# Performance work log

Hardware: AMD Instinct MI355X
Metric: run time of the kernel (lower is better)

## Reference

```python
import jax, jax.numpy as jnp
import numpy as np

L, H, M, KB = 8, 512, 32, 256  # layers, hidden, fourier modes, key bits
EPS = 1e-5


def setup_inputs() -> dict:
    key = jax.random.key(0)
    ks = jax.random.split(key, 20)
    B, S = 8, 2048
    s = 0.02
    return {
        'x': jax.random.normal(ks[0], (B, S), jnp.float32),
        # input projection Linear(1, H): weight [H] (squeezed), bias [H]
        'in_w': jax.random.normal(ks[1], (H,), jnp.float32) * s,
        'in_b': jax.random.normal(ks[2], (H,), jnp.float32) * s,
        # per-layer fourier weights (complex, stored as real/imag), conv1d(k=1), layernorm
        'fw_r': jax.random.normal(ks[3], (L, M, H, H), jnp.float32) * s,
        'fw_i': jax.random.normal(ks[4], (L, M, H, H), jnp.float32) * s,
        'conv_w': jax.random.normal(ks[5], (L, H, H), jnp.float32) / np.sqrt(H),
        'conv_b': jax.random.normal(ks[6], (L, H), jnp.float32) * s,
        'ln_g': jnp.ones((L, H), jnp.float32),
        'ln_b': jnp.zeros((L, H), jnp.float32),
        # output projection H -> H/2 -> H/4 -> 1
        'op1_w': jax.random.normal(ks[7], (H // 2, H), jnp.float32) / np.sqrt(H),
        'op1_b': jnp.zeros((H // 2,), jnp.float32),
        'op2_w': jax.random.normal(ks[8], (H // 4, H // 2), jnp.float32) / np.sqrt(H // 2),
        'op2_b': jnp.zeros((H // 4,), jnp.float32),
        'op3_w': jax.random.normal(ks[9], (1, H // 4), jnp.float32) / np.sqrt(H // 4),
        'op3_b': jnp.zeros((1,), jnp.float32),
        # cryptanalytic head H -> H -> KB (sigmoid)
        'h1_w': jax.random.normal(ks[10], (H, H), jnp.float32) / np.sqrt(H),
        'h1_b': jnp.zeros((H,), jnp.float32),
        'h2_w': jax.random.normal(ks[11], (KB, H), jnp.float32) / np.sqrt(H),
        'h2_b': jnp.zeros((KB,), jnp.float32),
    }


def _gelu(x):
    return jax.nn.gelu(x, approximate=False)


def _fourier_layer(x, Wc, cw, cb, g, b):
    # x: [B, S, H]; Wc: [M, H, H] complex
    S = x.shape[1]
    x_ft = jnp.fft.rfft(x, axis=1)  # [B, F, H] complex, F = S//2+1
    m = min(M, x_ft.shape[1])
    # batched per-mode complex GEMM (replaces python loop over modes)
    spec = jnp.einsum('bmh,mhk->bmk', x_ft[:, :m], Wc[:m])
    out_ft = jnp.concatenate([spec, jnp.zeros_like(x_ft[:, m:])], axis=1)
    x_fourier = jnp.fft.irfft(out_ft, n=S, axis=1)  # real [B, S, H]
    x_conv = x @ cw.T + cb  # Conv1d kernel-size-1 == per-position linear
    y = x_fourier + x_conv
    mu = jnp.mean(y, axis=-1, keepdims=True)
    var = jnp.var(y, axis=-1, keepdims=True)
    return (y - mu) * jax.lax.rsqrt(var + EPS) * g + b


def reference(x, in_w, in_b, fw_r, fw_i, conv_w, conv_b, ln_g, ln_b,
              op1_w, op1_b, op2_w, op2_b, op3_w, op3_b,
              h1_w, h1_b, h2_w, h2_b):
    # input projection: Linear(1, H) on x[..., None]
    h = x[:, :, None] * in_w[None, None, :] + in_b  # [B, S, H]
    Wc = fw_r + 1j * fw_i  # [L, M, H, H]
    for l in range(L):
        h = _fourier_layer(h, Wc[l], conv_w[l], conv_b[l], ln_g[l], ln_b[l]) + h
    # output projection (dropout is identity in eval)
    o = _gelu(h @ op1_w.T + op1_b)
    o = _gelu(o @ op2_w.T + op2_b)
    output = (o @ op3_w.T + op3_b)[..., 0]  # [B, S]
    gf = jnp.mean(h, axis=1)  # [B, H]
    k = _gelu(gf @ h1_w.T + h1_b)
    key_pred = jax.nn.sigmoid(k @ h2_w.T + h2_b)  # [B, KB]
    return output, key_pred
```

## Files before the change

### kernel.cpp

```cpp
#include <hip/hip_runtime.h>
#include <hip/hip_bf16.h>
#include <math.h>

#define BB   8
#define SEQ  2048
#define HD   512
#define LAY  8
#define MD   32
#define NKB  256
#define LNEPS 1e-5f

typedef __attribute__((ext_vector_type(8))) short v8s;
typedef __attribute__((ext_vector_type(4))) float v4f;
typedef __attribute__((ext_vector_type(4))) unsigned short v4us;

__device__ __forceinline__ float b2f(__hip_bfloat16 v) { return __bfloat162float(v); }
__device__ __forceinline__ float geluf(float v) { return v * 0.5f * (1.f + erff(v * 0.70710678118654752f)); }
__device__ __forceinline__ float bflo(unsigned int u) { return __uint_as_float((u & 0xFFFFu) << 16); }
__device__ __forceinline__ float bfhi(unsigned int u) { return __uint_as_float(u & 0xFFFF0000u); }

__device__ __forceinline__ float ldin(const void* p, size_t i, int bf) {
    if (bf) return __bfloat162float(((const __hip_bfloat16*)p)[i]);
    return ((const float*)p)[i];
}
__device__ __forceinline__ void stout(void* p, size_t i, float v, int bf) {
    if (bf) ((__hip_bfloat16*)p)[i] = __float2bfloat16(v);
    else    ((float*)p)[i] = v;
}

__device__ __forceinline__ void gl2lds16(const void* g, void* l) {
    __builtin_amdgcn_global_load_lds((__attribute__((address_space(1))) void*)g,
                                     (__attribute__((address_space(3))) void*)l, 16, 0, 0);
}

__global__ void k_flag(const unsigned int* __restrict__ lng_bits, int* __restrict__ flag) {
    if (threadIdx.x == 0 && blockIdx.x == 0)
        *flag = (lng_bits[0] == 0x3F803F80u) ? 1 : 0;
}

__global__ void k_setup(const void* __restrict__ x, const void* __restrict__ in_w, const void* __restrict__ in_b,
                        const void* __restrict__ cw, const void* __restrict__ w1, const void* __restrict__ w2,
                        const void* __restrict__ h1w, const void* __restrict__ h2w,
                        __hip_bfloat16* __restrict__ Ffwd, __hip_bfloat16* __restrict__ T2,
                        __hip_bfloat16* __restrict__ cwbf, __hip_bfloat16* __restrict__ w1bf,
                        __hip_bfloat16* __restrict__ w2bf, float* __restrict__ h1T, float* __restrict__ h2T,
                        float* __restrict__ h, __hip_bfloat16* __restrict__ hbf,
                        float* __restrict__ Xft, float* __restrict__ gf,
                        const int* __restrict__ flag) {
    int bf = *flag;
    int blk = blockIdx.x, t = threadIdx.x;
    if (blk < 512) {
        int idx = blk * 256 + t;
        int j = idx >> 11, s = idx & 2047;
        int m = j >> 1;
        int phase = (m * s) & (SEQ - 1);
        float ang = (float)phase * (6.283185307179586f / (float)SEQ);
        Ffwd[idx] = __float2bfloat16((j & 1) ? -sinf(ang) : cosf(ang));
    } else if (blk < 1024) {
        int idx = (blk - 512) * 256 + t;
        int s = idx >> 6, j = idx & 63;
        int m = j >> 1;
        float v;
        if (j == 0)      v = 1.f / (float)SEQ;
        else if (j == 1) v = 0.f;
        else {
            int phase = (m * s) & (SEQ - 1);
            float ang = (float)phase * (6.283185307179586f / (float)SEQ);
            v = (j & 1) ? (-2.f / (float)SEQ) * sinf(ang) : (2.f / (float)SEQ) * cosf(ang);
        }
        T2[idx] = __float2bfloat16(v);
    } else if (blk < 9216) {
        int idx = (blk - 1024) * 256 + t;
        cwbf[idx] = __float2bfloat16(ldin(cw, idx, bf));
    } else if (blk < 9728) {
        int idx = (blk - 9216) * 256 + t;
        w1bf[idx] = __float2bfloat16(ldin(w1, idx, bf));
    } else if (blk < 9856) {
        int idx = (blk - 9728) * 256 + t;
        w2bf[idx] = __float2bfloat16(ldin(w2, idx, bf));
    } else if (blk < 10880) {
        int idx = (blk - 9856) * 256 + t;
        int r = idx & 511, c = idx >> 9;
        h1T[idx] = ldin(h1w, (size_t)r * 512 + c, bf);
    } else if (blk < 11392) {
        int idx = (blk - 10880) * 256 + t;
        int r = idx & 255, c = idx >> 8;
        h2T[idx] = ldin(h2w, (size_t)r * 512 + c, bf);
    } else if (blk < 12416) {
        int idx = (blk - 11392) * 256 + t;
        Xft[idx] = 0.f;
    } else if (blk < 12432) {
        int idx = (blk - 12416) * 256 + t;
        gf[idx] = 0.f;
    } else {
        int idx = (blk - 12432) * 256 + t;
        int j = idx & 511;
        int bs = idx >> 9;
        float v = ldin(x, bs, bf) * ldin(in_w, j, bf) + ldin(in_b, j, bf);
        h[idx] = v;
        hbf[idx] = __float2bfloat16(v);
    }
}

__global__ __launch_bounds__(256) void k_fdft2(const __hip_bfloat16* __restrict__ hbf,
                                               const __hip_bfloat16* __restrict__ Ffwd,
                                               float* __restrict__ Xft) {
    __shared__ __align__(16) __hip_bfloat16 Als[2][16 * 72];
    int t = threadIdx.x;
    int lane = t & 63, wv = t >> 6;
    int ln15 = lane & 15, quad = lane >> 4;
    int ht = blockIdx.x, b = blockIdx.y, kh = blockIdx.z;
    int kcs = kh * 16;
    int sr = t >> 2, hc = (t & 3) * 4;

    v4f acc = (v4f){0.f, 0.f, 0.f, 0.f};

    const __hip_bfloat16* asrc0 = hbf + (size_t)b * SEQ * HD + ht * 16;
    const __hip_bfloat16* fbase = Ffwd + (size_t)(wv * 16 + ln15) * SEQ + quad * 8;

    v4us cur = *(const v4us*)(asrc0 + (size_t)(kcs * 64 + sr) * HD + hc);
#pragma unroll
    for (int e = 0; e < 4; e++)
        Als[0][(hc + e) * 72 + sr] = ((const __hip_bfloat16*)&cur)[e];
    __syncthreads();
    for (int i = 0; i < 16; i++) {
        int buf = i & 1;
        v4us nxt = cur;
        if (i < 15)
            nxt = *(const v4us*)(asrc0 + (size_t)((kcs + i + 1) * 64 + sr) * HD + hc);
        v8s bf0 = *(const v8s*)(fbase + (kcs + i) * 64);
        v8s bf1 = *(const v8s*)(fbase + (kcs + i) * 64 + 32);
        v8s af0 = *(const v8s*)&Als[buf][ln15 * 72 + quad * 8];
        v8s af1 = *(const v8s*)&Als[buf][ln15 * 72 + 32 + quad * 8];
        acc = __builtin_amdgcn_mfma_f32_16x16x32_bf16(af0, bf0, acc, 0, 0, 0);
        acc = __builtin_amdgcn_mfma_f32_16x16x32_bf16(af1, bf1, acc, 0, 0, 0);
        if (i < 15) {
#pragma unroll
            for (int e = 0; e < 4; e++)
                Als[buf ^ 1][(hc + e) * 72 + sr] = ((const __hip_bfloat16*)&nxt)[e];
        }
        __syncthreads();
        cur = nxt;
    }
    int j = wv * 16 + ln15;
    int m = j >> 1, c = j & 1;
    int hg = ht * 16 + quad * 4;
#pragma unroll
    for (int r = 0; r < 4; r++)
        atomicAdd(&Xft[(size_t)(b * 32 + m) * 1024 + (size_t)(hg + r) * 2 + c], acc[r]);
}

__global__ __launch_bounds__(512) void k_mix(const float* __restrict__ Xft,
                                             const void* __restrict__ fwr, const void* __restrict__ fwi,
                                             __hip_bfloat16* __restrict__ spec2, int l,
                                             const int* __restrict__ flag) {
    int bf = *flag;
    int kt = blockIdx.x;
    int m  = blockIdx.y;
    int t = threadIdx.x;
    int kl = t & 15, hg = t >> 4;
    int k0 = kt * 64 + kl * 4;
    __shared__ float xs[8192];
    __shared__ float red[32 * 512];
    for (int e = t; e < 8192; e += 512) {
        int bb = e >> 10, r = e & 1023;
        xs[bb * 1024 + r] = Xft[(size_t)(bb * 32 + m) * 1024 + r];
    }
    __syncthreads();
    float ar[8][4], ai[8][4];
#pragma unroll
    for (int bb = 0; bb < 8; bb++)
#pragma unroll
        for (int q = 0; q < 4; q++) { ar[bb][q] = 0.f; ai[bb][q] = 0.f; }
    size_t wbase = (size_t)(l * 32 + m) * 262144 + k0;
    const float2* xs2 = (const float2*)xs;
    if (bf) {
        const __hip_bfloat16* fr = (const __hip_bfloat16*)fwr;
        const __hip_bfloat16* fi = (const __hip_bfloat16*)fwi;
        for (int hh = hg; hh < 512; hh += 32) {
            v4us urv = *(const v4us*)(fr + wbase + (size_t)hh * 512);
            v4us uiv = *(const v4us*)(fi + wbase + (size_t)hh * 512);
            float wr[4], wi[4];
#pragma unroll
            for (int q = 0; q < 4; q++) {
                wr[q] = __uint_as_float(((unsigned int)(unsigned short)urv[q]) << 16);
                wi[q] = __uint_as_float(((unsigned int)(unsigned short)uiv[q]) << 16);
            }
#pragma unroll
            for (int bb = 0; bb < 8; bb++) {
                float2 x2 = xs2[bb * 512 + hh];
#pragma unroll
                for (int q = 0; q < 4; q++) {
                    ar[bb][q] += x2.x * wr[q] - x2.y * wi[q];
                    ai[bb][q] += x2.x * wi[q] + x2.y * wr[q];
                }
            }
        }
    } else {
        const float* fr = (const float*)fwr;
        const float* fi = (const float*)fwi;
        for (int hh = hg; hh < 512; hh += 32) {
            v4f wrv = *(const v4f*)(fr + wbase + (size_t)hh * 512);
            v4f wiv = *(const v4f*)(fi + wbase + (size_t)hh * 512);
#pragma unroll
            for (int bb = 0; bb < 8; bb++) {
                float2 x2 = xs2[bb * 512 + hh];
#pragma unroll
                for (int q = 0; q < 4; q++) {
                    ar[bb][q] += x2.x * wrv[q] - x2.y * wiv[q];
                    ai[bb][q] += x2.x * wiv[q] + x2.y * wrv[q];
                }
            }
        }
    }
    v4f* red4 = (v4f*)red;
#pragma unroll
    for (int bb = 0; bb < 8; bb++)
        red4[hg * 128 + bb * 16 + kl] = (v4f){ar[bb][0], ar[bb][1], ar[bb][2], ar[bb][3]};
    __syncthreads();
    float sr = 0.f;
#pragma unroll
    for (int g = 0; g < 32; g++) sr += red[g * 512 + t];
    __syncthreads();
#pragma unroll
    for (int bb = 0; bb < 8; bb++)
        red4[hg * 128 + bb * 16 + kl] = (v4f){ai[bb][0], ai[bb][1], ai[bb][2], ai[bb][3]};
    __syncthreads();
    float si = 0.f;
#pragma unroll
    for (int g = 0; g < 32; g++) si += red[g * 512 + t];

    int bb = t >> 6, j = t & 63;
    int k = kt * 64 + j;
    size_t o = ((size_t)(bb * 512 + k) << 6) + 2 * m;
    __hip_bfloat16 hr = __float2bfloat16(sr), hi = __float2bfloat16(si);
    unsigned int pk = (unsigned int)*(unsigned short*)&hr | ((unsigned int)*(unsigned short*)&hi << 16);
    *(unsigned int*)(spec2 + o) = pk;
}

__global__ __launch_bounds__(512) void k_gln(__hip_bfloat16* __restrict__ hbf,
                                             const __hip_bfloat16* __restrict__ cwbf,
                                             const __hip_bfloat16* __restrict__ T2,
                                             const __hip_bfloat16* __restrict__ spec2,
                                             const void* __restrict__ cb,
                                             const void* __restrict__ lng, const void* __restrict__ lnb,
                                             float* __restrict__ h,
                                             float* __restrict__ Xft,
                                             int l, const int* __restrict__ flag) {
    int bfv = *flag;
    __shared__ __align__(16) __hip_bfloat16 smem[64 * 520];
    __shared__ float stats[128];
    __hip_bfloat16* Als = smem;
    __hip_bfloat16* Bls = smem + 2048;
    __hip_bfloat16* Yls = smem;

    int t = threadIdx.x;
    int lane = t & 63, wv = t >> 6;
    int wr = wv >> 2, wc = wv & 3;
    int ln15 = lane & 15, quad = lane >> 4;
    int row0 = blockIdx.x * 64;
    int b = row0 >> 11, s0 = row0 & 2047;

    {
        float* xz = Xft + (size_t)blockIdx.x * 1024;
        xz[t] = 0.f; xz[t + 512] = 0.f;
    }

    v4f acc[16];
#pragma unroll
    for (int i = 0; i < 16; i++) acc[i] = (v4f){0.f, 0.f, 0.f, 0.f};

    const __hip_bfloat16* cwl = cwbf + (size_t)l * 262144;
    for (int kc = 0; kc < 18; kc++) {
        int k0 = kc * 32;
        if (t < 256) {
            int row = t >> 2, kq = (t & 3) * 8;
            const __hip_bfloat16* asrc = (k0 < 512)
                ? hbf + (size_t)(row0 + row) * 512 + k0 + kq
                : T2 + (size_t)(s0 + row) * 64 + (k0 - 512) + kq;
            gl2lds16(asrc, &Als[(size_t)(wv * 64) * 8]);
        }
#pragma unroll
        for (int p = 0; p < 4; p++) {
            int i = p * 512 + t;
            int n = i >> 2, kq = (i & 3) * 8;
            const __hip_bfloat16* bsrc = (k0 < 512)
                ? cwl + (size_t)n * 512 + k0 + kq
                : spec2 + (size_t)(b * 512 + n) * 64 + (k0 - 512) + kq;
            gl2lds16(bsrc, &Bls[(size_t)(p * 512 + wv * 64) * 8]);
        }
        __syncthreads();
        v8s af[2], bfr[8];
#pragma unroll
        for (int i = 0; i < 2; i++)
            af[i] = *(const v8s*)&Als[(wr * 32 + i * 16 + ln15) * 32 + quad * 8];
#pragma unroll
        for (int j = 0; j < 8; j++)
            bfr[j] = *(const v8s*)&Bls[(wc * 128 + j * 16 + ln15) * 32 + quad * 8];
#pragma unroll
        for (int i = 0; i < 2; i++)
#pragma unroll
            for (int j = 0; j < 8; j++)
                acc[i * 8 + j] = __builtin_amdgcn_mfma_f32_16x16x32_bf16(af[i], bfr[j], acc[i * 8 + j], 0, 0, 0);
        __syncthreads();
    }
#pragma unroll
    for (int j = 0; j < 8; j++) {
        int col = wc * 128 + j * 16 + ln15;
        float cbv = ldin(cb, l * HD + col, bfv);
#pragma unroll
        for (int i = 0; i < 2; i++) {
            int rl = wr * 32 + i * 16 + quad * 4;
#pragma unroll
            for (int r = 0; r < 4; r++)
                Yls[(rl + r) * 520 + col] = __float2bfloat16(acc[i * 8 + j][r] + cbv);
        }
    }
    __syncthreads();
    {
        int r = t >> 3, g = t & 7;
        float s = 0.f, q = 0.f;
        for (int i = 0; i < 32; i++) {
            int cp = g + i * 8;
            unsigned int u = *(const unsigned int*)&Yls[r * 520 + cp * 2];
            float v0 = bflo(u), v1 = bfhi(u);
            s += v0 + v1; q += v0 * v0 + v1 * v1;
        }
        s += __shfl_xor(s, 1); s += __shfl_xor(s, 2); s += __shfl_xor(s, 4);
        q += __shfl_xor(q, 1); q += __shfl_xor(q, 2); q += __shfl_xor(q, 4);
        if (g == 0) {
            float mu = s * (1.f / (float)HD);
            float var = q * (1.f / (float)HD) - mu * mu;
            stats[r * 2] = mu; stats[r * 2 + 1] = rsqrtf(var + LNEPS);
        }
    }
    __syncthreads();
    for (int k = 0; k < 32; k++) {
        int e2 = t + 512 * k;
        int r = e2 >> 8, c2 = e2 & 255;
        float mu = stats[r * 2], rs = stats[r * 2 + 1];
        unsigned int u = *(const unsigned int*)&Yls[r * 520 + c2 * 2];
        float v0 = bflo(u), v1 = bfhi(u);
        int gc = 2 * c2;
        float g0 = ldin(lng, l * HD + gc, bfv),     g1 = ldin(lng, l * HD + gc + 1, bfv);
        float b0 = ldin(lnb, l * HD + gc, bfv),     b1 = ldin(lnb, l * HD + gc + 1, bfv);
        float2 hv = *(const float2*)&h[(size_t)(row0 + r) * HD + gc];
        float n0 = (v0 - mu) * rs * g0 + b0 + hv.x;
        float n1 = (v1 - mu) * rs * g1 + b1 + hv.y;
        *(float2*)&h[(size_t)(row0 + r) * HD + gc] = (float2){n0, n1};
        __hip_bfloat16 a0 = __float2bfloat16(n0), a1 = __float2bfloat16(n1);
        unsigned int up = ((unsigned int)(*(unsigned short*)&a1) << 16) | (unsigned int)(*(unsigned short*)&a0);
        ((unsigned int*)(hbf + (size_t)(row0 + r) * HD))[c2] = up;
    }
}

__global__ __launch_bounds__(256) void k_pj1(const __hip_bfloat16* __restrict__ hbf,
                                             const __hip_bfloat16* __restrict__ w1bf,
                                             const void* __restrict__ b1,
                                             __hip_bfloat16* __restrict__ o1bf,
                                             const int* __restrict__ flag) {
    int bfv = *flag;
    __shared__ __hip_bfloat16 Als[128 * 32];
    __shared__ __hip_bfloat16 Bls[128 * 32];
    int t = threadIdx.x;
    int lane = t & 63, wv = t >> 6;
    int wr = wv >> 1, wc = wv & 1;
    int ln15 = lane & 15, quad = lane >> 4;
    int row0 = blockIdx.x * 128, n0 = blockIdx.y * 128;

    v4f acc[16];
#pragma unroll
    for (int i = 0; i < 16; i++) acc[i] = (v4f){0.f, 0.f, 0.f, 0.f};

    for (int kc = 0; kc < 16; kc++) {
        int k0 = kc * 32;
#pragma unroll
        for (int p = 0; p < 2; p++) {
            int i = p * 256 + t;
            int row = i >> 2, kq = (i & 3) * 8;
            gl2lds16(hbf + (size_t)(row0 + row) * 512 + k0 + kq, &Als[(size_t)(p * 256 + wv * 64) * 8]);
            gl2lds16(w1bf + (size_t)(n0 + row) * 512 + k0 + kq, &Bls[(size_t)(p * 256 + wv * 64) * 8]);
        }
        __syncthreads();
        v8s af[4], bfr[4];
#pragma unroll
        for (int i = 0; i < 4; i++)
            af[i] = *(const v8s*)&Als[(wr * 64 + i * 16 + ln15) * 32 + quad * 8];
#pragma unroll
        for (int j = 0; j < 4; j++)
            bfr[j] = *(const v8s*)&Bls[(wc * 64 + j * 16 + ln15) * 32 + quad * 8];
#pragma unroll
        for (int i = 0; i < 4; i++)
#pragma unroll
            for (int j = 0; j < 4; j++)
                acc[i * 4 + j] = __builtin_amdgcn_mfma_f32_16x16x32_bf16(af[i], bfr[j], acc[i * 4 + j], 0, 0, 0);
        __syncthreads();
    }
#pragma unroll
    for (int j = 0; j < 4; j++) {
        int col = n0 + wc * 64 + j * 16 + ln15;
        float bv = ldin(b1, col, bfv);
#pragma unroll
        for (int i = 0; i < 4; i++) {
            int rg = row0 + wr * 64 + i * 16 + quad * 4;
#pragma unroll
            for (int r = 0; r < 4; r++)
                o1bf[(size_t)(rg + r) * 256 + col] = __float2bfloat16(geluf(acc[i * 4 + j][r] + bv));
        }
    }
}

__global__ __launch_bounds__(256) void k_pj2(const __hip_bfloat16* __restrict__ o1bf,
                                             const __hip_bfloat16* __restrict__ w2bf,
                                             const void* __restrict__ b2,
                                             const void* __restrict__ w3, const void* __restrict__ b3,
                                             void* __restrict__ out, const int* __restrict__ flag) {
    int bfv = *flag;
    __shared__ __hip_bfloat16 Als[128 * 32];
    __shared__ __hip_bfloat16 Bls[128 * 32];
    __shared__ __hip_bfloat16 o2s[128 * 130];
    __shared__ float w3s[128];
    int t = threadIdx.x;
    int lane = t & 63, wv = t >> 6;
    int wr = wv >> 1, wc = wv & 1;
    int ln15 = lane & 15, quad = lane >> 4;
    int row0 = blockIdx.x * 128;
    if (t < 128) w3s[t] = ldin(w3, t, bfv);

    v4f acc[16];
#pragma unroll
    for (int i = 0; i < 16; i++) acc[i] = (v4f){0.f, 0.f, 0.f, 0.f};

    for (int kc = 0; kc < 8; kc++) {
        int k0 = kc * 32;
#pragma unroll
        for (int p = 0; p < 2; p++) {
            int i = p * 256 + t;
            int row = i >> 2, kq = (i & 3) * 8;
            gl2lds16(o1bf + (size_t)(row0 + row) * 256 + k0 + kq, &Als[(size_t)(p * 256 + wv * 64) * 8]);
            gl2lds16(w2bf + (size_t)row * 256 + k0 + kq,          &Bls[(size_t)(p * 256 + wv * 64) * 8]);
        }
        __syncthreads();
        v8s af[4], bfr[4];
#pragma unroll
        for (int i = 0; i < 4; i++)
            af[i] = *(const v8s*)&Als[(wr * 64 + i * 16 + ln15) * 32 + quad * 8];
#pragma unroll
        for (int j = 0; j < 4; j++)
            bfr[j] = *(const v8s*)&Bls[(wc * 64 + j * 16 + ln15) * 32 + quad * 8];
#pragma unroll
        for (int i = 0; i < 4; i++)
#pragma unroll
            for (int j = 0; j < 4; j++)
                acc[i * 4 + j] = __builtin_amdgcn_mfma_f32_16x16x32_bf16(af[i], bfr[j], acc[i * 4 + j], 0, 0, 0);
        __syncthreads();
    }
#pragma unroll
    for (int j = 0; j < 4; j++) {
        int col = wc * 64 + j * 16 + ln15;
        float bv = ldin(b2, col, bfv);
#pragma unroll
        for (int i = 0; i < 4; i++) {
            int rl = wr * 64 + i * 16 + quad * 4;
#pragma unroll
            for (int r = 0; r < 4; r++)
                o2s[(rl + r) * 130 + col] = __float2bfloat16(geluf(acc[i * 4 + j][r] + bv));
        }
    }
    __syncthreads();
    if (t < 128) {
        float s = 0.f;
        for (int j = 0; j < 128; j++) s += b2f(o2s[t * 130 + j]) * w3s[j];
        stout(out, row0 + t, s + ldin(b3, 0, bfv), bfv);
    }
}

__global__ __launch_bounds__(512) void k_gf(const float* __restrict__ h, float* __restrict__ gf) {
    int sc = blockIdx.x, b = blockIdx.y;
    int j = threadIdx.x;
    const float* p = h + ((size_t)b * SEQ + sc * 64) * HD + j;
    float s = 0.f;
    for (int i = 0; i < 64; i++) s += p[(size_t)i * HD];
    atomicAdd(&gf[b * HD + j], s * (1.f / (float)SEQ));
}

__global__ __launch_bounds__(512) void k_head(const float* __restrict__ gf,
                                              const float* __restrict__ h1T, const void* __restrict__ h1b,
                                              const float* __restrict__ h2T, const void* __restrict__ h2b,
                                              void* __restrict__ out, const int* __restrict__ flag) {
    int bf = *flag;
    int b = blockIdx.x;
    int t = threadIdx.x;
    __shared__ float gs[512];
    __shared__ float ks[512];
    gs[t] = gf[b * HD + t];
    __syncthreads();
    float a = 0.f;
    for (int j = 0; j < 512; j++) a += gs[j] * h1T[j * 512 + t];
    ks[t] = geluf(a + ldin(h1b, t, bf));
    __syncthreads();
    if (t < 256) {
        float s = 0.f;
        for (int j = 0; j < 512; j++) s += ks[j] * h2T[j * 256 + t];
        s += ldin(h2b, t, bf);
        stout(out, BB * SEQ + b * NKB + t, 1.f / (1.f + expf(-s)), bf);
    }
}

extern "C" void kernel_launch(void* const* d_in, const int* in_sizes, int n_in,
                              void* d_out, int out_size, void* d_ws, size_t ws_size,
                              hipStream_t stream) {
    const void* x    = d_in[0];
    const void* in_w = d_in[1];
    const void* in_b = d_in[2];
    const void* fwr  = d_in[3];
    const void* fwi  = d_in[4];
    const void* cw   = d_in[5];
    const void* cb   = d_in[6];
    const void* lng  = d_in[7];
    const void* lnb  = d_in[8];
    const void* w1   = d_in[9];
    const void* b1   = d_in[10];
    const void* w2   = d_in[11];
    const void* b2   = d_in[12];
    const void* w3   = d_in[13];
    const void* b3   = d_in[14];
    const void* h1w  = d_in[15];
    const void* h1b  = d_in[16];
    const void* h2w  = d_in[17];
    const void* h2b  = d_in[18];

    float* ws = (float*)d_ws;
    __hip_bfloat16* Ffwd = (__hip_bfloat16*)ws;
    float*          h    = ws + 131072;
    float*          Xp   = h + 8388608;
    __hip_bfloat16* o1bf = (__hip_bfloat16*)Xp;
    __hip_bfloat16* hbf  = (__hip_bfloat16*)(Xp + 4194304);
    __hip_bfloat16* cwbf = (__hip_bfloat16*)(Xp + 8388608);
    __hip_bfloat16* T2   = (__hip_bfloat16*)(Xp + 10485760);
    __hip_bfloat16* spec2= (__hip_bfloat16*)(Xp + 10551296);
    float*          Xft  = Xp + 10682368;
    float*          gf   = Xft + 262144;
    float*          w1T  = gf + 4096;
    __hip_bfloat16* w1bf = (__hip_bfloat16*)w1T;
    __hip_bfloat16* w2bf = (__hip_bfloat16*)(w1T + 65536);
    float*          w2T  = w1T + 131072;
    float*          h1T  = w2T + 32768;
    float*          h2T  = h1T + 262144;
    int*            flag = (int*)(h2T + 131072);

    k_flag<<<1, 1, 0, stream>>>((const unsigned int*)lng, flag);
    k_setup<<<45200, 256, 0, stream>>>(x, in_w, in_b, cw, w1, w2, h1w, h2w,
                                       Ffwd, T2, cwbf, w1bf, w2bf, h1T, h2T,
                                       h, hbf, Xft, gf, flag);

    for (int l = 0; l < LAY; l++) {
        k_fdft2<<<dim3(32, 8, 2), 256, 0, stream>>>(hbf, Ffwd, Xft);
        k_mix<<<dim3(8, 32), 512, 0, stream>>>(Xft, fwr, fwi, spec2, l, flag);
        k_gln<<<256, 512, 0, stream>>>(hbf, cwbf, T2, spec2, cb, lng, lnb, h, Xft, l, flag);
    }

    k_gf<<<dim3(32, 8), 512, 0, stream>>>(h, gf);
    k_pj1<<<dim3(128, 2), 256, 0, stream>>>(hbf, w1bf, b1, o1bf, flag);
    k_pj2<<<128, 256, 0, stream>>>(o1bf, w2bf, b2, w3, b3, d_out, flag);
    k_head<<<8, 512, 0, stream>>>(gf, h1T, h1b, h2T, h2b, d_out, flag);
}
```

Measured before the change: 1.209 ms.

## Double-buffer GEMM LDS stages, replace DFT atomics with split partials

The forward-DFT kernel now writes its two K-half results into separate partial buffers, which the mix kernel sums. This removes the atomicAdds and the per-layer zeroing of Xft in k_gln and setup. k_gln, k_pj1 and k_pj2 switch to double-buffered LDS so the next K-chunk's global-to-LDS load overlaps the current MFMAs. k_mix loops get unroll 2, and the layernorm epilogue hoists the gamma/beta loads out of its row loop. Double-buffering raises LDS use per block, which can lower occupancy, especially in k_gln.

```diff
diff --git a/kernel.cpp b/kernel.cpp
--- a/kernel.cpp
+++ b/kernel.cpp
@@ -45,7 +45,7 @@
                         __hip_bfloat16* __restrict__ cwbf, __hip_bfloat16* __restrict__ w1bf,
                         __hip_bfloat16* __restrict__ w2bf, float* __restrict__ h1T, float* __restrict__ h2T,
                         float* __restrict__ h, __hip_bfloat16* __restrict__ hbf,
-                        float* __restrict__ Xft, float* __restrict__ gf,
+                        float* __restrict__ gf,
                         const int* __restrict__ flag) {
     int bf = *flag;
     int blk = blockIdx.x, t = threadIdx.x;
@@ -86,14 +86,11 @@
         int idx = (blk - 10880) * 256 + t;
         int r = idx & 255, c = idx >> 8;
         h2T[idx] = ldin(h2w, (size_t)r * 512 + c, bf);
-    } else if (blk < 12416) {
+    } else if (blk < 11408) {
         int idx = (blk - 11392) * 256 + t;
-        Xft[idx] = 0.f;
-    } else if (blk < 12432) {
-        int idx = (blk - 12416) * 256 + t;
         gf[idx] = 0.f;
     } else {
-        int idx = (blk - 12432) * 256 + t;
+        int idx = (blk - 11408) * 256 + t;
         int j = idx & 511;
         int bs = idx >> 9;
         float v = ldin(x, bs, bf) * ldin(in_w, j, bf) + ldin(in_b, j, bf);
@@ -104,7 +101,7 @@
 
 __global__ __launch_bounds__(256) void k_fdft2(const __hip_bfloat16* __restrict__ hbf,
                                                const __hip_bfloat16* __restrict__ Ffwd,
-                                               float* __restrict__ Xft) {
+                                               float* __restrict__ Xpart) {
     __shared__ __align__(16) __hip_bfloat16 Als[2][16 * 72];
     int t = threadIdx.x;
     int lane = t & 63, wv = t >> 6;
@@ -145,12 +142,13 @@
     int j = wv * 16 + ln15;
     int m = j >> 1, c = j & 1;
     int hg = ht * 16 + quad * 4;
+    float* outp = Xpart + (size_t)kh * 262144 + (size_t)(b * 32 + m) * 1024;
 #pragma unroll
     for (int r = 0; r < 4; r++)
-        atomicAdd(&Xft[(size_t)(b * 32 + m) * 1024 + (size_t)(hg + r) * 2 + c], acc[r]);
-}
-
-__global__ __launch_bounds__(512) void k_mix(const float* __restrict__ Xft,
+        outp[(size_t)(hg + r) * 2 + c] = acc[r];
+}
+
+__global__ __launch_bounds__(512) void k_mix(const float* __restrict__ Xp0, const float* __restrict__ Xp1,
                                              const void* __restrict__ fwr, const void* __restrict__ fwi,
                                              __hip_bfloat16* __restrict__ spec2, int l,
                                              const int* __restrict__ flag) {
@@ -164,7 +162,8 @@
     __shared__ float red[32 * 512];
     for (int e = t; e < 8192; e += 512) {
         int bb = e >> 10, r = e & 1023;
-        xs[bb * 1024 + r] = Xft[(size_t)(bb * 32 + m) * 1024 + r];
+        size_t off = (size_t)(bb * 32 + m) * 1024 + r;
+        xs[bb * 1024 + r] = Xp0[off] + Xp1[off];
     }
     __syncthreads();
     float ar[8][4], ai[8][4];
@@ -177,6 +176,7 @@
     if (bf) {
         const __hip_bfloat16* fr = (const __hip_bfloat16*)fwr;
         const __hip_bfloat16* fi = (const __hip_bfloat16*)fwi;
+#pragma unroll 2
         for (int hh = hg; hh < 512; hh += 32) {
             v4us urv = *(const v4us*)(fr + wbase + (size_t)hh * 512);
             v4us uiv = *(const v4us*)(fi + wbase + (size_t)hh * 512);
@@ -199,6 +199,7 @@
     } else {
         const float* fr = (const float*)fwr;
         const float* fi = (const float*)fwi;
+#pragma unroll 2
         for (int hh = hg; hh < 512; hh += 32) {
             v4f wrv = *(const v4f*)(fr + wbase + (size_t)hh * 512);
             v4f wiv = *(const v4f*)(fi + wbase + (size_t)hh * 512);
@@ -245,14 +246,11 @@
                                              const void* __restrict__ cb,
                                              const void* __restrict__ lng, const void* __restrict__ lnb,
                                              float* __restrict__ h,
-                                             float* __restrict__ Xft,
                                              int l, const int* __restrict__ flag) {
     int bfv = *flag;
-    __shared__ __align__(16) __hip_bfloat16 smem[64 * 520];
+    __shared__ __align__(16) __hip_bfloat16 smem[2][18432];
     __shared__ float stats[128];
-    __hip_bfloat16* Als = smem;
-    __hip_bfloat16* Bls = smem + 2048;
-    __hip_bfloat16* Yls = smem;
+    __hip_bfloat16* Yls = &smem[0][0];
 
     int t = threadIdx.x;
     int lane = t & 63, wv = t >> 6;
@@ -261,24 +259,20 @@
     int row0 = blockIdx.x * 64;
     int b = row0 >> 11, s0 = row0 & 2047;
 
-    {
-        float* xz = Xft + (size_t)blockIdx.x * 1024;
-        xz[t] = 0.f; xz[t + 512] = 0.f;
-    }
-
     v4f acc[16];
 #pragma unroll
     for (int i = 0; i < 16; i++) acc[i] = (v4f){0.f, 0.f, 0.f, 0.f};
 
     const __hip_bfloat16* cwl = cwbf + (size_t)l * 262144;
-    for (int kc = 0; kc < 18; kc++) {
+
+    auto stage = [&](int buf, int kc) {
         int k0 = kc * 32;
         if (t < 256) {
             int row = t >> 2, kq = (t & 3) * 8;
             const __hip_bfloat16* asrc = (k0 < 512)
                 ? hbf + (size_t)(row0 + row) * 512 + k0 + kq
                 : T2 + (size_t)(s0 + row) * 64 + (k0 - 512) + kq;
-            gl2lds16(asrc, &Als[(size_t)(wv * 64) * 8]);
+            gl2lds16(asrc, &smem[buf][(size_t)(wv * 64) * 8]);
         }
 #pragma unroll
         for (int p = 0; p < 4; p++) {
@@ -287,9 +281,17 @@
             const __hip_bfloat16* bsrc = (k0 < 512)
                 ? cwl + (size_t)n * 512 + k0 + kq
                 : spec2 + (size_t)(b * 512 + n) * 64 + (k0 - 512) + kq;
-            gl2lds16(bsrc, &Bls[(size_t)(p * 512 + wv * 64) * 8]);
-        }
-        __syncthreads();
+            gl2lds16(bsrc, &smem[buf][2048 + (size_t)(p * 512 + wv * 64) * 8]);
+        }
+    };
+
+    stage(0, 0);
+    __syncthreads();
+    int cur = 0;
+    for (int kc = 0; kc < 18; kc++) {
+        if (kc < 17) stage(cur ^ 1, kc + 1);
+        const __hip_bfloat16* Als = &smem[cur][0];
+        const __hip_bfloat16* Bls = &smem[cur][2048];
         v8s af[2], bfr[8];
 #pragma unroll
         for (int i = 0; i < 2; i++)
@@ -303,6 +305,7 @@
             for (int j = 0; j < 8; j++)
                 acc[i * 8 + j] = __builtin_amdgcn_mfma_f32_16x16x32_bf16(af[i], bfr[j], acc[i * 8 + j], 0, 0, 0);
         __syncthreads();
+        cur ^= 1;
     }
 #pragma unroll
     for (int j = 0; j < 8; j++) {
@@ -335,22 +338,25 @@
         }
     }
     __syncthreads();
-    for (int k = 0; k < 32; k++) {
-        int e2 = t + 512 * k;
-        int r = e2 >> 8, c2 = e2 & 255;
-        float mu = stats[r * 2], rs = stats[r * 2 + 1];
-        unsigned int u = *(const unsigned int*)&Yls[r * 520 + c2 * 2];
-        float v0 = bflo(u), v1 = bfhi(u);
+    {
+        int c2 = t & 255;
         int gc = 2 * c2;
         float g0 = ldin(lng, l * HD + gc, bfv),     g1 = ldin(lng, l * HD + gc + 1, bfv);
         float b0 = ldin(lnb, l * HD + gc, bfv),     b1 = ldin(lnb, l * HD + gc + 1, bfv);
-        float2 hv = *(const float2*)&h[(size_t)(row0 + r) * HD + gc];
-        float n0 = (v0 - mu) * rs * g0 + b0 + hv.x;
-        float n1 = (v1 - mu) * rs * g1 + b1 + hv.y;
-        *(float2*)&h[(size_t)(row0 + r) * HD + gc] = (float2){n0, n1};
-        __hip_bfloat16 a0 = __float2bfloat16(n0), a1 = __float2bfloat16(n1);
-        unsigned int up = ((unsigned int)(*(unsigned short*)&a1) << 16) | (unsigned int)(*(unsigned short*)&a0);
-        ((unsigned int*)(hbf + (size_t)(row0 + r) * HD))[c2] = up;
+        int rbase = t >> 8;
+        for (int k = 0; k < 32; k++) {
+            int r = rbase + 2 * k;
+            float mu = stats[r * 2], rs = stats[r * 2 + 1];
+            unsigned int u = *(const unsigned int*)&Yls[r * 520 + c2 * 2];
+            float v0 = bflo(u), v1 = bfhi(u);
+            float2 hv = *(const float2*)&h[(size_t)(row0 + r) * HD + gc];
+            float n0 = (v0 - mu) * rs * g0 + b0 + hv.x;
+            float n1 = (v1 - mu) * rs * g1 + b1 + hv.y;
+            *(float2*)&h[(size_t)(row0 + r) * HD + gc] = (float2){n0, n1};
+            __hip_bfloat16 a0 = __float2bfloat16(n0), a1 = __float2bfloat16(n1);
+            unsigned int up = ((unsigned int)(*(unsigned short*)&a1) << 16) | (unsigned int)(*(unsigned short*)&a0);
+            ((unsigned int*)(hbf + (size_t)(row0 + r) * HD))[c2] = up;
+        }
     }
 }
 
@@ -360,8 +366,7 @@
                                              __hip_bfloat16* __restrict__ o1bf,
                                              const int* __restrict__ flag) {
     int bfv = *flag;
-    __shared__ __hip_bfloat16 Als[128 * 32];
-    __shared__ __hip_bfloat16 Bls[128 * 32];
+    __shared__ __align__(16) __hip_bfloat16 smem[2][8192];
     int t = threadIdx.x;
     int lane = t & 63, wv = t >> 6;
     int wr = wv >> 1, wc = wv & 1;
@@ -372,16 +377,24 @@
 #pragma unroll
     for (int i = 0; i < 16; i++) acc[i] = (v4f){0.f, 0.f, 0.f, 0.f};
 
-    for (int kc = 0; kc < 16; kc++) {
+    auto stage = [&](int buf, int kc) {
         int k0 = kc * 32;
 #pragma unroll
         for (int p = 0; p < 2; p++) {
             int i = p * 256 + t;
             int row = i >> 2, kq = (i & 3) * 8;
-            gl2lds16(hbf + (size_t)(row0 + row) * 512 + k0 + kq, &Als[(size_t)(p * 256 + wv * 64) * 8]);
-            gl2lds16(w1bf + (size_t)(n0 + row) * 512 + k0 + kq, &Bls[(size_t)(p * 256 + wv * 64) * 8]);
-        }
-        __syncthreads();
+            gl2lds16(hbf + (size_t)(row0 + row) * 512 + k0 + kq, &smem[buf][(size_t)(p * 256 + wv * 64) * 8]);
+            gl2lds16(w1bf + (size_t)(n0 + row) * 512 + k0 + kq, &smem[buf][4096 + (size_t)(p * 256 + wv * 64) * 8]);
+        }
+    };
+
+    stage(0, 0);
+    __syncthreads();
+    int cur = 0;
+    for (int kc = 0; kc < 16; kc++) {
+        if (kc < 15) stage(cur ^ 1, kc + 1);
+        const __hip_bfloat16* Als = &smem[cur][0];
+        const __hip_bfloat16* Bls = &smem[cur][4096];
         v8s af[4], bfr[4];
 #pragma unroll
         for (int i = 0; i < 4; i++)
@@ -395,6 +408,7 @@
             for (int j = 0; j < 4; j++)
                 acc[i * 4 + j] = __builtin_amdgcn_mfma_f32_16x16x32_bf16(af[i], bfr[j], acc[i * 4 + j], 0, 0, 0);
         __syncthreads();
+        cur ^= 1;
     }
 #pragma unroll
     for (int j = 0; j < 4; j++) {
@@ -416,8 +430,7 @@
                                              const void* __restrict__ w3, const void* __restrict__ b3,
                                              void* __restrict__ out, const int* __restrict__ flag) {
     int bfv = *flag;
-    __shared__ __hip_bfloat16 Als[128 * 32];
-    __shared__ __hip_bfloat16 Bls[128 * 32];
+    __shared__ __align__(16) __hip_bfloat16 smem[2][8192];
     __shared__ __hip_bfloat16 o2s[128 * 130];
     __shared__ float w3s[128];
     int t = threadIdx.x;
@@ -431,16 +444,24 @@
 #pragma unroll
     for (int i = 0; i < 16; i++) acc[i] = (v4f){0.f, 0.f, 0.f, 0.f};
 
-    for (int kc = 0; kc < 8; kc++) {
+    auto stage = [&](int buf, int kc) {
         int k0 = kc * 32;
 #pragma unroll
         for (int p = 0; p < 2; p++) {
             int i = p * 256 + t;
             int row = i >> 2, kq = (i & 3) * 8;
-            gl2lds16(o1bf + (size_t)(row0 + row) * 256 + k0 + kq, &Als[(size_t)(p * 256 + wv * 64) * 8]);
-            gl2lds16(w2bf + (size_t)row * 256 + k0 + kq,          &Bls[(size_t)(p * 256 + wv * 64) * 8]);
-        }
-        __syncthreads();
+            gl2lds16(o1bf + (size_t)(row0 + row) * 256 + k0 + kq, &smem[buf][(size_t)(p * 256 + wv * 64) * 8]);
+            gl2lds16(w2bf + (size_t)row * 256 + k0 + kq,          &smem[buf][4096 + (size_t)(p * 256 + wv * 64) * 8]);
+        }
+    };
+
+    stage(0, 0);
+    __syncthreads();
+    int cur = 0;
+    for (int kc = 0; kc < 8; kc++) {
+        if (kc < 7) stage(cur ^ 1, kc + 1);
+        const __hip_bfloat16* Als = &smem[cur][0];
+        const __hip_bfloat16* Bls = &smem[cur][4096];
         v8s af[4], bfr[4];
 #pragma unroll
         for (int i = 0; i < 4; i++)
@@ -454,6 +475,7 @@
             for (int j = 0; j < 4; j++)
                 acc[i * 4 + j] = __builtin_amdgcn_mfma_f32_16x16x32_bf16(af[i], bfr[j], acc[i * 4 + j], 0, 0, 0);
         __syncthreads();
+        cur ^= 1;
     }
 #pragma unroll
     for (int j = 0; j < 4; j++) {
@@ -539,8 +561,8 @@
     __hip_bfloat16* cwbf = (__hip_bfloat16*)(Xp + 8388608);
     __hip_bfloat16* T2   = (__hip_bfloat16*)(Xp + 10485760);
     __hip_bfloat16* spec2= (__hip_bfloat16*)(Xp + 10551296);
-    float*          Xft  = Xp + 10682368;
-    float*          gf   = Xft + 262144;
+    float*          XftOld = Xp + 10682368;
+    float*          gf   = XftOld + 262144;
     float*          w1T  = gf + 4096;
     __hip_bfloat16* w1bf = (__hip_bfloat16*)w1T;
     __hip_bfloat16* w2bf = (__hip_bfloat16*)(w1T + 65536);
@@ -548,16 +570,17 @@
     float*          h1T  = w2T + 32768;
     float*          h2T  = h1T + 262144;
     int*            flag = (int*)(h2T + 131072);
+    float*          Xpart = h2T + 131072 + 64;
 
     k_flag<<<1, 1, 0, stream>>>((const unsigned int*)lng, flag);
-    k_setup<<<45200, 256, 0, stream>>>(x, in_w, in_b, cw, w1, w2, h1w, h2w,
+    k_setup<<<44176, 256, 0, stream>>>(x, in_w, in_b, cw, w1, w2, h1w, h2w,
                                        Ffwd, T2, cwbf, w1bf, w2bf, h1T, h2T,
-                                       h, hbf, Xft, gf, flag);
+                                       h, hbf, gf, flag);
 
     for (int l = 0; l < LAY; l++) {
-        k_fdft2<<<dim3(32, 8, 2), 256, 0, stream>>>(hbf, Ffwd, Xft);
-        k_mix<<<dim3(8, 32), 512, 0, stream>>>(Xft, fwr, fwi, spec2, l, flag);
-        k_gln<<<256, 512, 0, stream>>>(hbf, cwbf, T2, spec2, cb, lng, lnb, h, Xft, l, flag);
+        k_fdft2<<<dim3(32, 8, 2), 256, 0, stream>>>(hbf, Ffwd, Xpart);
+        k_mix<<<dim3(8, 32), 512, 0, stream>>>(Xpart, Xpart + 262144, fwr, fwi, spec2, l, flag);
+        k_gln<<<256, 512, 0, stream>>>(hbf, cwbf, T2, spec2, cb, lng, lnb, h, l, flag);
     }
 
     k_gf<<<dim3(32, 8), 512, 0, stream>>>(h, gf);
```

After: 1.189 ms. No clear change (-1.7%).
